# Performance work log

Measured on AMD Instinct MI355X. Metric: run time of the kernel, lower is better.

The kernel has to match this reference:

```python
import jax, jax.numpy as jnp
import numpy as np

B, H, S, DK, DV = 4, 16, 2048, 64, 64

def setup_inputs() -> dict:
    key = jax.random.key(0)
    k1, k2, k3, k4 = jax.random.split(key, 4)
    Q = jax.random.normal(k1, (B, H, S, DK), dtype=jnp.float32)
    K = jax.random.normal(k2, (B, H, S, DK), dtype=jnp.float32)
    V = jax.random.normal(k3, (B, H, S, DV), dtype=jnp.float32)
    mask_out = jax.random.randint(k4, (B, 1, 1, S), 0, 2).astype(jnp.bool_)
    return {"Q": Q, "K": K, "V": V, "mask_out": mask_out}

def reference(Q, K, V, mask_out):
    key_size = Q.shape[-1]
    seq_q, seq_k = Q.shape[-2], K.shape[-2]
    scale = jnp.sqrt(jnp.float32(key_size))
    # scores: [B, H, Sq, Sk]
    scores = jnp.einsum('bhqd,bhkd->bhqk', Q, K) / scale
    scores = jnp.where(mask_out, jnp.float32(-1e9), scores)
    attn = jax.nn.softmax(scores, axis=-1)
    # Gaussian relative-position decay: exp(-|i-j|^2 / (Sk^2 / 2))
    idx_q = jnp.arange(seq_q, dtype=jnp.float32)[:, None]
    idx_k = jnp.arange(seq_k, dtype=jnp.float32)[None, :]
    rel = idx_q - idx_k  # [Sq, Sk]
    decay = jnp.exp(-(rel * rel) * (2.0 / (seq_k * seq_k)))  # [Sq, Sk]
    attn = attn * decay  # broadcast over [B, H]
    return jnp.einsum('bhqk,bhkv->bhqv', attn, V)
```

## Files before the change

kernel.cpp:

```cpp
#include <hip/hip_runtime.h>
#include <hip/hip_bf16.h>
#include <hip/hip_fp16.h>

typedef __attribute__((ext_vector_type(8))) short bf16x8;
typedef __attribute__((ext_vector_type(4))) short bf16x4;
typedef __attribute__((ext_vector_type(4))) float f32x4;
typedef __attribute__((ext_vector_type(4))) unsigned u32x4;
typedef __attribute__((ext_vector_type(4))) int i32x4;

constexpr int Bn = 4, Hn = 16, S = 2048, D = 64;
constexpr int BQ = 128;
constexpr float LOG2E = 1.44269504088896340736f;
constexpr float CD2f = (2.0f / ((float)S * (float)S)) * LOG2E;

__device__ __forceinline__ unsigned cvtpk(float lo, float hi) {
    unsigned r;
    asm("v_cvt_pk_bf16_f32 %0, %1, %2" : "=v"(r) : "v"(lo), "v"(hi));
    return r;
}

__device__ __forceinline__ f32x4 mfma16(bf16x4 a, bf16x4 b, f32x4 c) {
#if __has_builtin(__builtin_amdgcn_mfma_f32_16x16x16bf16_1k)
    return __builtin_amdgcn_mfma_f32_16x16x16bf16_1k(a, b, c, 0, 0, 0);
#else
    asm volatile("v_mfma_f32_16x16x16_bf16 %0, %1, %2, %0"
                 : "+v"(c) : "v"(a), "v"(b));
    return c;
#endif
}

__device__ __forceinline__ void gload16(const short* g, short* lds) {
    __builtin_amdgcn_global_load_lds(
        (const __attribute__((address_space(1))) unsigned*)g,
        (__attribute__((address_space(3))) unsigned*)lds,
        16, 0, 0);
}

__global__ void compact_mask(const void* __restrict__ maskg,
                             int* __restrict__ idxp, int* __restrict__ Mg) {
    const int b = blockIdx.x, t = threadIdx.x;
    __shared__ int wsum[4];
    __shared__ int Msh;

    const unsigned* mu = (const unsigned*)maskg;
    bool is_bytes = false;
    #pragma unroll 8
    for (int i = 0; i < 64; ++i) is_bytes |= (mu[i] > 1u);

    int keep[8]; int cnt = 0;
    #pragma unroll
    for (int i = 0; i < 8; ++i) {
        const int key = t * 8 + i;
        int m;
        if (is_bytes) m = ((const unsigned char*)maskg)[b * S + key];
        else          m = ((const int*)maskg)[b * S + key];
        keep[i] = (m == 0);
        cnt += keep[i];
    }
    const int l = t & 63, w = t >> 6;
    int pre = cnt;
    #pragma unroll
    for (int d = 1; d < 64; d <<= 1) {
        int v = __shfl_up(pre, d, 64);
        if (l >= d) pre += v;
    }
    if (l == 63) wsum[w] = pre;
    __syncthreads();
    int base = 0;
    for (int i = 0; i < w; ++i) base += wsum[i];
    int offs = base + pre - cnt;
    #pragma unroll
    for (int i = 0; i < 8; ++i)
        if (keep[i]) idxp[b * S + (offs++)] = t * 8 + i;
    if (t == 255) Msh = base + pre;
    __syncthreads();
    const int M = Msh;
    for (int i = M + t; i < S; i += 256) idxp[b * S + i] = 0;
    if (M == 0)
        for (int i = t; i < S; i += 256) idxp[b * S + i] = i;
    if (t == 0) Mg[b] = (M == 0) ? -1 : M;
}

__global__ void pack_kv(const float* __restrict__ Kg, const float* __restrict__ Vg,
                        const int* __restrict__ idxp, const int* __restrict__ Mg,
                        short* __restrict__ Kw, short* __restrict__ Vw) {
    const int bh = blockIdx.x, b = bh >> 4;
    const int ck0 = blockIdx.y * 256;
    const int t = threadIdx.x;
    const int Mraw = Mg[b];
    const int M = (Mraw < 0) ? S : Mraw;
    if (ck0 >= M) return;
    const int* idxb = idxp + b * S;
    const float* Kp = Kg + (size_t)bh * S * D;
    const float* Vp = Vg + (size_t)bh * S * D;

    {
        const int dc = (t & 7) * 8;
        #pragma unroll
        for (int tile = 0; tile < 4; ++tile)
            #pragma unroll
            for (int it = 0; it < 2; ++it) {
                const int key = ck0 + tile * 64 + (t >> 3) + it * 32;
                u32x4 pk = u32x4{0u, 0u, 0u, 0u};
                if (key < M) {
                    const float* src = Kp + (size_t)idxb[key] * D + dc;
                    #pragma unroll
                    for (int jj = 0; jj < 4; ++jj)
                        pk[jj] = cvtpk(src[2 * jj], src[2 * jj + 1]);
                }
                *(u32x4*)(Kw + ((size_t)bh * S + key) * D + dc) = pk;
            }
    }
    {
        const int dv = t & 63;
        const int kb = (t >> 6) * 16;
        #pragma unroll
        for (int tile = 0; tile < 4; ++tile) {
            const int tg = (ck0 >> 6) + tile;
            float f[16];
            #pragma unroll
            for (int i = 0; i < 16; ++i) {
                const int key = ck0 + tile * 64 + kb + i;
                float v = 0.f;
                if (key < M) {
                    int row = idxb[key];
                    row = __builtin_amdgcn_readfirstlane(row);
                    v = Vp[(size_t)row * D + dv];
                }
                f[i] = v;
            }
            u32x4 p0, p1;
            #pragma unroll
            for (int jj = 0; jj < 4; ++jj) {
                p0[jj] = cvtpk(f[2 * jj], f[2 * jj + 1]);
                p1[jj] = cvtpk(f[8 + 2 * jj], f[9 + 2 * jj]);
            }
            short* dst = Vw + (((size_t)bh * 32 + tg) * 64 + dv) * 64 + kb;
            *(u32x4*)dst = p0;
            *(u32x4*)(dst + 8) = p1;
        }
    }
}

__global__ __launch_bounds__(256, 4) void attn_packed(
    const float* __restrict__ Qg, const short* __restrict__ Kw,
    const short* __restrict__ Vw, const int* __restrict__ idxp,
    const int* __restrict__ Mg, float* __restrict__ outg)
{
    __shared__ alignas(16) short Kt[2][64][64];
    __shared__ alignas(16) short Vt[2][64][64];
    __shared__ alignas(16) __half dtab[2176];

    const int bid  = blockIdx.x;
    const int lblk = ((bid & 7) << 7) | (bid >> 3);
    const int qt   = lblk & 15;
    const int bh   = lblk >> 4;
    const int b    = bh >> 4;
    const int q0   = qt * BQ;

    const float* Qp   = Qg + ((size_t)bh * S + q0) * D;
    const short* Ksrc = Kw + (size_t)bh * S * D;
    const short* Vsrc = Vw + (size_t)bh * 32 * 64 * 64;
    float*       Op   = outg + ((size_t)bh * S + q0) * D;
    const int*   idxb = idxp + b * S;

    const int t  = threadIdx.x;
    const int w  = t >> 6;
    const int l  = t & 63;
    const int lr = l & 15;
    const int lg = l >> 4;
    const int lx = lr & 7;

    const int  Mraw    = Mg[b];
    const bool uniform = (Mraw < 0);
    const int  M       = uniform ? S : Mraw;
    const int  ntiles  = (M + 63) >> 6;

    int so[2], ld[2];
    #pragma unroll
    for (int p = 0; p < 2; ++p) {
        const int r = (p * 4 + w) * 8 + (l >> 3);
        so[p] = r * 64 + (((l & 7) ^ (r & 7)) << 3);
        ld[p] = (p * 4 + w) * 512;
    }

    gload16(Ksrc + so[0], &Kt[0][0][0] + ld[0]);
    gload16(Ksrc + so[1], &Kt[0][0][0] + ld[1]);
    gload16(Vsrc + so[0], &Vt[0][0][0] + ld[0]);
    gload16(Vsrc + so[1], &Vt[0][0][0] + ld[1]);

    for (int i = t; i < 2176; i += 256) {
        const float r = (float)(q0 + i - 2047);
        dtab[i] = __float2half(__builtin_exp2f(-CD2f * r * r));
    }

    const float qscale = uniform ? 0.0f : 0.125f * LOG2E;
    bf16x8 qf[2][2];
    #pragma unroll
    for (int rt = 0; rt < 2; ++rt) {
        const int row = w * 32 + rt * 16 + lr;
        #pragma unroll
        for (int g = 0; g < 2; ++g) {
            const float* src = Qp + row * D + g * 32 + lg * 8;
            union { unsigned u[4]; bf16x8 v; } cv;
            #pragma unroll
            for (int jj = 0; jj < 4; ++jj)
                cv.u[jj] = cvtpk(src[2 * jj] * qscale, src[2 * jj + 1] * qscale);
            qf[rt][g] = cv.v;
        }
    }

    f32x4 Oacc[2][4];
    #pragma unroll
    for (int rt = 0; rt < 2; ++rt)
        #pragma unroll
        for (int dt = 0; dt < 4; ++dt) Oacc[rt][dt] = f32x4{0.f, 0.f, 0.f, 0.f};
    float lrun[2] = {0.f, 0.f};

    const int qi0 = w * 32 + lr + 2047;

    asm volatile("s_waitcnt vmcnt(0)" ::: "memory");
    __syncthreads();

    int c = 0;
    for (int tt = 0; tt < ntiles; ++tt) {
        const int  rem  = M - tt * 64;
        const bool last = (rem <= 64);

        if (tt + 1 < ntiles) {
            const short* kp = Ksrc + (size_t)(tt + 1) * 4096;
            const short* vp = Vsrc + (size_t)(tt + 1) * 4096;
            gload16(kp + so[0], &Kt[c ^ 1][0][0] + ld[0]);
            gload16(kp + so[1], &Kt[c ^ 1][0][0] + ld[1]);
            gload16(vp + so[0], &Vt[c ^ 1][0][0] + ld[0]);
            gload16(vp + so[1], &Vt[c ^ 1][0][0] + ld[1]);
        }

        const char* kbase = (const char*)&Kt[c][0][0];
        const char* vbase = (const char*)&Vt[c][0][0];

        #pragma unroll
        for (int kt = 0; kt < 4; ++kt) {
            const bf16x8 kf0 = *(const bf16x8*)(kbase + (kt * 16 + lr) * 128
                                                + ((lg ^ lx) << 4));
            const bf16x8 kf1 = *(const bf16x8*)(kbase + (kt * 16 + lr) * 128
                                                + (((4 + lg) ^ lx) << 4));
            f32x4 s0 = f32x4{-16.f, -16.f, -16.f, -16.f};
            f32x4 s1 = f32x4{-16.f, -16.f, -16.f, -16.f};
            __builtin_amdgcn_s_setprio(1);
            s0 = __builtin_amdgcn_mfma_f32_16x16x32_bf16(kf0, qf[0][0], s0, 0, 0, 0);
            s0 = __builtin_amdgcn_mfma_f32_16x16x32_bf16(kf1, qf[0][1], s0, 0, 0, 0);
            s1 = __builtin_amdgcn_mfma_f32_16x16x32_bf16(kf0, qf[1][0], s1, 0, 0, 0);
            s1 = __builtin_amdgcn_mfma_f32_16x16x32_bf16(kf1, qf[1][1], s1, 0, 0, 0);
            __builtin_amdgcn_s_setprio(0);

            const i32x4 iv = *(const i32x4*)(idxb + tt * 64 + kt * 16 + lg * 4);

            bf16x4 Xb[2];
            #pragma unroll
            for (int rt = 0; rt < 2; ++rt) {
                const f32x4 s = rt ? s1 : s0;
                float p0 = __builtin_exp2f(s[0]);
                float p1 = __builtin_exp2f(s[1]);
                float p2 = __builtin_exp2f(s[2]);
                float p3 = __builtin_exp2f(s[3]);
                if (last) {
                    const int ck = kt * 16 + lg * 4;
                    p0 = (ck + 0 < rem) ? p0 : 0.f;
                    p1 = (ck + 1 < rem) ? p1 : 0.f;
                    p2 = (ck + 2 < rem) ? p2 : 0.f;
                    p3 = (ck + 3 < rem) ? p3 : 0.f;
                }
                lrun[rt] += (p0 + p1) + (p2 + p3);
                const int qi = qi0 + rt * 16;
                const float d0 = __half2float(dtab[qi - iv[0]]);
                const float d1 = __half2float(dtab[qi - iv[1]]);
                const float d2 = __half2float(dtab[qi - iv[2]]);
                const float d3 = __half2float(dtab[qi - iv[3]]);
                union { unsigned u[2]; bf16x4 v; } cx;
                cx.u[0] = cvtpk(p0 * d0, p1 * d1);
                cx.u[1] = cvtpk(p2 * d2, p3 * d3);
                Xb[rt] = cx.v;
            }

            __builtin_amdgcn_s_setprio(1);
            #pragma unroll
            for (int dt = 0; dt < 4; ++dt) {
                const bf16x4 vA = *(const bf16x4*)(vbase + (dt * 16 + lr) * 128
                          + ((((2 * kt + (lg >> 1)) ^ lx) << 4) | ((lg & 1) << 3)));
                Oacc[0][dt] = mfma16(vA, Xb[0], Oacc[0][dt]);
                Oacc[1][dt] = mfma16(vA, Xb[1], Oacc[1][dt]);
            }
            __builtin_amdgcn_s_setprio(0);
        }

        asm volatile("s_waitcnt vmcnt(0)" ::: "memory");
        __syncthreads();
        c ^= 1;
    }

    #pragma unroll
    for (int rt = 0; rt < 2; ++rt) {
        float ls = lrun[rt];
        ls += __shfl_xor(ls, 16, 64);
        ls += __shfl_xor(ls, 32, 64);
        const float inv = 1.0f / ls;
        const int row = w * 32 + rt * 16 + lr;
        #pragma unroll
        for (int dt = 0; dt < 4; ++dt) {
            f32x4 o = Oacc[rt][dt];
            o[0] *= inv; o[1] *= inv; o[2] *= inv; o[3] *= inv;
            *(f32x4*)&Op[(size_t)row * D + dt * 16 + lg * 4] = o;
        }
    }
}

__global__ __launch_bounds__(256, 3) void attn_gather(
    const float* __restrict__ Qg, const float* __restrict__ Kg,
    const float* __restrict__ Vg, const int* __restrict__ idxp,
    const int* __restrict__ Mg, float* __restrict__ outg)
{
    __shared__ alignas(16) short Kt[64][72];
    __shared__ alignas(16) short Vt[64][72];
    __shared__ alignas(16) float dtab[2176];
    __shared__ alignas(16) int   idxs[64];

    const int blk = blockIdx.x;
    const int qt  = blk & 15;
    const int bh  = blk >> 4;
    const int b   = bh >> 4;
    const int q0  = qt * BQ;

    const float* Qp = Qg + ((size_t)bh * S + q0) * D;
    const float* Kp = Kg + (size_t)bh * S * D;
    const float* Vp = Vg + (size_t)bh * S * D;
    float*       Op = outg + ((size_t)bh * S + q0) * D;
    const int*   idxb = idxp + b * S;

    const int t  = threadIdx.x;
    const int w  = t >> 6;
    const int l  = t & 63;
    const int lr = l & 15;
    const int lg = l >> 4;

    const int  Mraw    = Mg[b];
    const bool uniform = (Mraw < 0);
    const int  M       = uniform ? S : Mraw;

    for (int i = t; i < 2176; i += 256) {
        const float r = (float)(q0 + i - 2047);
        dtab[i] = __builtin_exp2f(-CD2f * r * r);
    }

    const float qscale = uniform ? 0.0f : 0.125f * LOG2E;
    bf16x8 qf[2][2];
    #pragma unroll
    for (int rt = 0; rt < 2; ++rt) {
        const int row = w * 32 + rt * 16 + lr;
        #pragma unroll
        for (int g = 0; g < 2; ++g) {
            const float* src = Qp + row * D + g * 32 + lg * 8;
            union { unsigned u[4]; bf16x8 v; } cv;
            #pragma unroll
            for (int jj = 0; jj < 4; ++jj)
                cv.u[jj] = cvtpk(src[2 * jj] * qscale, src[2 * jj + 1] * qscale);
            qf[rt][g] = cv.v;
        }
    }

    f32x4 Oacc[2][4];
    #pragma unroll
    for (int rt = 0; rt < 2; ++rt)
        #pragma unroll
        for (int dt = 0; dt < 4; ++dt) Oacc[rt][dt] = f32x4{0.f, 0.f, 0.f, 0.f};
    float lrun[2] = {0.f, 0.f};

    const int qrl2047 = w * 32 + lr + 2047;

    for (int kv = 0; kv < M; kv += 64) {
        const int  rem  = M - kv;
        const bool last = (rem <= 64);
        __syncthreads();
        {
            const int key = t >> 3;
            const int dc  = (t & 7) * 8;
            #pragma unroll
            for (int it = 0; it < 2; ++it) {
                const int row = idxb[kv + key + it * 32];
                const float* src = Kp + (size_t)row * D + dc;
                u32x4 pk;
                #pragma unroll
                for (int jj = 0; jj < 4; ++jj)
                    pk[jj] = cvtpk(src[2 * jj], src[2 * jj + 1]);
                *(u32x4*)&Kt[key + it * 32][dc] = pk;
            }
        }
        if (t < 64) idxs[t] = idxb[kv + t];
        {
            const int dv = t & 63;
            const int kb = (t >> 6) * 16;
            float f[16];
            #pragma unroll
            for (int i = 0; i < 16; ++i) {
                int row = idxb[kv + kb + i];
                row = __builtin_amdgcn_readfirstlane(row);
                f[i] = Vp[(size_t)row * D + dv];
            }
            u32x4 p0, p1;
            #pragma unroll
            for (int jj = 0; jj < 4; ++jj) {
                p0[jj] = cvtpk(f[2 * jj], f[2 * jj + 1]);
                p1[jj] = cvtpk(f[8 + 2 * jj], f[9 + 2 * jj]);
            }
            *(u32x4*)&Vt[dv][kb]     = p0;
            *(u32x4*)&Vt[dv][kb + 8] = p1;
        }
        __syncthreads();

        bf16x8 kf[4][2];
        #pragma unroll
        for (int kt = 0; kt < 4; ++kt)
            #pragma unroll
            for (int g = 0; g < 2; ++g)
                kf[kt][g] = *(const bf16x8*)&Kt[kt * 16 + lr][g * 32 + lg * 8];

        bf16x4 Xb[2][4];
        #pragma unroll
        for (int rt = 0; rt < 2; ++rt) {
            f32x4 sc[4];
            #pragma unroll
            for (int kt = 0; kt < 4; ++kt) {
                f32x4 acc = f32x4{-16.f, -16.f, -16.f, -16.f};
                acc = __builtin_amdgcn_mfma_f32_16x16x32_bf16(kf[kt][0], qf[rt][0], acc, 0, 0, 0);
                acc = __builtin_amdgcn_mfma_f32_16x16x32_bf16(kf[kt][1], qf[rt][1], acc, 0, 0, 0);
                sc[kt] = acc;
            }
            const int qi = qrl2047 + rt * 16;
            float lp = 0.f;
            #pragma unroll
            for (int kt = 0; kt < 4; ++kt) {
                const i32x4 iv = *(const i32x4*)&idxs[kt * 16 + lg * 4];
                float p0 = __builtin_exp2f(sc[kt][0]);
                float p1 = __builtin_exp2f(sc[kt][1]);
                float p2 = __builtin_exp2f(sc[kt][2]);
                float p3 = __builtin_exp2f(sc[kt][3]);
                if (last) {
                    const int ck = kt * 16 + lg * 4;
                    p0 = (ck + 0 < rem) ? p0 : 0.f;
                    p1 = (ck + 1 < rem) ? p1 : 0.f;
                    p2 = (ck + 2 < rem) ? p2 : 0.f;
                    p3 = (ck + 3 < rem) ? p3 : 0.f;
                }
                lp += (p0 + p1) + (p2 + p3);
                const float d0 = dtab[qi - iv[0]];
                const float d1 = dtab[qi - iv[1]];
                const float d2 = dtab[qi - iv[2]];
                const float d3 = dtab[qi - iv[3]];
                union { unsigned u[2]; bf16x4 v; } cx;
                cx.u[0] = cvtpk(p0 * d0, p1 * d1);
                cx.u[1] = cvtpk(p2 * d2, p3 * d3);
                Xb[rt][kt] = cx.v;
            }
            lrun[rt] += lp;
        }

        #pragma unroll
        for (int kt = 0; kt < 4; ++kt) {
            bf16x4 vA[4];
            #pragma unroll
            for (int dt = 0; dt < 4; ++dt)
                vA[dt] = *(const bf16x4*)&Vt[dt * 16 + lr][kt * 16 + lg * 4];
            #pragma unroll
            for (int dt = 0; dt < 4; ++dt) {
                Oacc[0][dt] = mfma16(vA[dt], Xb[0][kt], Oacc[0][dt]);
                Oacc[1][dt] = mfma16(vA[dt], Xb[1][kt], Oacc[1][dt]);
            }
        }
    }

    #pragma unroll
    for (int rt = 0; rt < 2; ++rt) {
        float ls = lrun[rt];
        ls += __shfl_xor(ls, 16, 64);
        ls += __shfl_xor(ls, 32, 64);
        const float inv = 1.0f / ls;
        const int row = w * 32 + rt * 16 + lr;
        #pragma unroll
        for (int dt = 0; dt < 4; ++dt) {
            f32x4 o = Oacc[rt][dt];
            o[0] *= inv; o[1] *= inv; o[2] *= inv; o[3] *= inv;
            *(f32x4*)&Op[(size_t)row * D + dt * 16 + lg * 4] = o;
        }
    }
}

extern "C" void kernel_launch(void* const* d_in, const int* in_sizes, int n_in,
                              void* d_out, int out_size, void* d_ws, size_t ws_size,
                              hipStream_t stream) {
    const float* Q = (const float*)d_in[0];
    const float* K = (const float*)d_in[1];
    const float* V = (const float*)d_in[2];
    const void*  M = d_in[3];
    float* out = (float*)d_out;

    int* idxp = (int*)d_ws;
    int* Mg   = idxp + Bn * S;
    size_t base = (((size_t)(Bn * S + Bn) * 4) + 255) & ~(size_t)255;
    short* Kw = (short*)((char*)d_ws + base);
    short* Vw = Kw + (size_t)Bn * Hn * S * D;
    const size_t need = base + 2 * (size_t)Bn * Hn * S * D * sizeof(short);

    compact_mask<<<dim3(Bn), dim3(256), 0, stream>>>(M, idxp, Mg);
    const int nblk = Bn * Hn * (S / BQ);
    if (ws_size >= need) {
        pack_kv<<<dim3(Bn * Hn, S / 256), dim3(256), 0, stream>>>(K, V, idxp, Mg, Kw, Vw);
        attn_packed<<<dim3(nblk), dim3(256), 0, stream>>>(Q, Kw, Vw, idxp, Mg, out);
    } else {
        attn_gather<<<dim3(nblk), dim3(256), 0, stream>>>(Q, K, V, idxp, Mg, out);
    }
}
```

Baseline: 119.0 us.

## Prefetch key indices and decay table values ahead of use; halve pack_kv chunk

The attention loop now loads the next tile's compacted key indices during the current tile. It also gathers the Gaussian decay values from the fp16 table into registers ahead of the MFMA work, in two halves, so that global/L2 gather latency is hidden behind the score matmuls. Separately, pack_kv processes 128 keys per block instead of 256 and launches twice as many blocks, giving more parallelism for the gather/convert step. The prefetching adds register pressure, which may lower occupancy.

```diff
diff --git a/kernel.cpp b/kernel.cpp
--- a/kernel.cpp
+++ b/kernel.cpp
@@ -85,7 +85,7 @@
                         const int* __restrict__ idxp, const int* __restrict__ Mg,
                         short* __restrict__ Kw, short* __restrict__ Vw) {
     const int bh = blockIdx.x, b = bh >> 4;
-    const int ck0 = blockIdx.y * 256;
+    const int ck0 = blockIdx.y * 128;
     const int t = threadIdx.x;
     const int Mraw = Mg[b];
     const int M = (Mraw < 0) ? S : Mraw;
@@ -97,7 +97,7 @@
     {
         const int dc = (t & 7) * 8;
         #pragma unroll
-        for (int tile = 0; tile < 4; ++tile)
+        for (int tile = 0; tile < 2; ++tile)
             #pragma unroll
             for (int it = 0; it < 2; ++it) {
                 const int key = ck0 + tile * 64 + (t >> 3) + it * 32;
@@ -115,7 +115,7 @@
         const int dv = t & 63;
         const int kb = (t >> 6) * 16;
         #pragma unroll
-        for (int tile = 0; tile < 4; ++tile) {
+        for (int tile = 0; tile < 2; ++tile) {
             const int tg = (ck0 >> 6) + tile;
             float f[16];
             #pragma unroll
@@ -217,17 +217,42 @@
         for (int dt = 0; dt < 4; ++dt) Oacc[rt][dt] = f32x4{0.f, 0.f, 0.f, 0.f};
     float lrun[2] = {0.f, 0.f};
 
-    const int qi0 = w * 32 + lr + 2047;
+    const int qiA = w * 32 + lr + 2047;
+    const int qiB = qiA + 16;
+
+    i32x4 ivc[4];
+    #pragma unroll
+    for (int kt = 0; kt < 4; ++kt)
+        ivc[kt] = *(const i32x4*)(idxb + kt * 16 + lg * 4);
 
     asm volatile("s_waitcnt vmcnt(0)" ::: "memory");
     __syncthreads();
 
     int c = 0;
     for (int tt = 0; tt < ntiles; ++tt) {
-        const int  rem  = M - tt * 64;
-        const bool last = (rem <= 64);
-
-        if (tt + 1 < ntiles) {
+        const int  rem      = M - tt * 64;
+        const bool last     = (rem <= 64);
+        const bool havenext = (tt + 1 < ntiles);
+
+        __half dpre[4][2][4];
+        #pragma unroll
+        for (int kt = 0; kt < 2; ++kt)
+            #pragma unroll
+            for (int e = 0; e < 4; ++e) {
+                dpre[kt][0][e] = dtab[qiA - ivc[kt][e]];
+                dpre[kt][1][e] = dtab[qiB - ivc[kt][e]];
+            }
+
+        i32x4 ivn[4];
+        #pragma unroll
+        for (int kt = 0; kt < 4; ++kt) ivn[kt] = ivc[kt];
+        if (havenext) {
+            #pragma unroll
+            for (int kt = 0; kt < 4; ++kt)
+                ivn[kt] = *(const i32x4*)(idxb + (tt + 1) * 64 + kt * 16 + lg * 4);
+        }
+
+        if (havenext) {
             const short* kp = Ksrc + (size_t)(tt + 1) * 4096;
             const short* vp = Vsrc + (size_t)(tt + 1) * 4096;
             gload16(kp + so[0], &Kt[c ^ 1][0][0] + ld[0]);
@@ -241,6 +266,15 @@
 
         #pragma unroll
         for (int kt = 0; kt < 4; ++kt) {
+            if (kt == 2) {
+                #pragma unroll
+                for (int k2 = 2; k2 < 4; ++k2)
+                    #pragma unroll
+                    for (int e = 0; e < 4; ++e) {
+                        dpre[k2][0][e] = dtab[qiA - ivc[k2][e]];
+                        dpre[k2][1][e] = dtab[qiB - ivc[k2][e]];
+                    }
+            }
             const bf16x8 kf0 = *(const bf16x8*)(kbase + (kt * 16 + lr) * 128
                                                 + ((lg ^ lx) << 4));
             const bf16x8 kf1 = *(const bf16x8*)(kbase + (kt * 16 + lr) * 128
@@ -253,8 +287,6 @@
             s1 = __builtin_amdgcn_mfma_f32_16x16x32_bf16(kf0, qf[1][0], s1, 0, 0, 0);
             s1 = __builtin_amdgcn_mfma_f32_16x16x32_bf16(kf1, qf[1][1], s1, 0, 0, 0);
             __builtin_amdgcn_s_setprio(0);
-
-            const i32x4 iv = *(const i32x4*)(idxb + tt * 64 + kt * 16 + lg * 4);
 
             bf16x4 Xb[2];
             #pragma unroll
@@ -272,11 +304,10 @@
                     p3 = (ck + 3 < rem) ? p3 : 0.f;
                 }
                 lrun[rt] += (p0 + p1) + (p2 + p3);
-                const int qi = qi0 + rt * 16;
-                const float d0 = __half2float(dtab[qi - iv[0]]);
-                const float d1 = __half2float(dtab[qi - iv[1]]);
-                const float d2 = __half2float(dtab[qi - iv[2]]);
-                const float d3 = __half2float(dtab[qi - iv[3]]);
+                const float d0 = __half2float(dpre[kt][rt][0]);
+                const float d1 = __half2float(dpre[kt][rt][1]);
+                const float d2 = __half2float(dpre[kt][rt][2]);
+                const float d3 = __half2float(dpre[kt][rt][3]);
                 union { unsigned u[2]; bf16x4 v; } cx;
                 cx.u[0] = cvtpk(p0 * d0, p1 * d1);
                 cx.u[1] = cvtpk(p2 * d2, p3 * d3);
@@ -293,6 +324,9 @@
             }
             __builtin_amdgcn_s_setprio(0);
         }
+
+        #pragma unroll
+        for (int kt = 0; kt < 4; ++kt) ivc[kt] = ivn[kt];
 
         asm volatile("s_waitcnt vmcnt(0)" ::: "memory");
         __syncthreads();
@@ -513,7 +547,7 @@
     compact_mask<<<dim3(Bn), dim3(256), 0, stream>>>(M, idxp, Mg);
     const int nblk = Bn * Hn * (S / BQ);
     if (ws_size >= need) {
-        pack_kv<<<dim3(Bn * Hn, S / 256), dim3(256), 0, stream>>>(K, V, idxp, Mg, Kw, Vw);
+        pack_kv<<<dim3(Bn * Hn, S / 128), dim3(256), 0, stream>>>(K, V, idxp, Mg, Kw, Vw);
         attn_packed<<<dim3(nblk), dim3(256), 0, stream>>>(Q, Kw, Vw, idxp, Mg, out);
     } else {
         attn_gather<<<dim3(nblk), dim3(256), 0, stream>>>(Q, K, V, idxp, Mg, out);
```

Result: slower. 188.5 us (+58.4%).
